# Optimization experiments

Measured on AMD Instinct MI355X. Metric: run time of the kernel, lower is better.

## Reference

```python
import jax, jax.numpy as jnp
import numpy as np

EPS_COS = 1e-8  # torch cosine_similarity eps
EPS_LN = 1e-5   # torch LayerNorm eps


def setup_inputs() -> dict:
    key = jax.random.key(0)
    ks = jax.random.split(key, 8)
    B, N, D, C = 256, 65536, 1024, 103
    s = 1.0 / np.sqrt(D)
    return {
        "visual_input": jnp.zeros((1,), jnp.float32),
        "query_input": jax.random.normal(ks[0], (B, D), jnp.float32),
        "memory_keys": jax.random.normal(ks[1], (N, D), jnp.float32),
        "W_enc": jax.random.normal(ks[2], (D, D), jnp.float32) * s,
        "b_enc": jnp.zeros((D,), jnp.float32),
        "W_d": jax.random.normal(ks[3], (D, D), jnp.float32) * s,
        "b_d": jnp.zeros((D,), jnp.float32),
        "ln_g": jnp.ones((D,), jnp.float32),
        "ln_b": jnp.zeros((D,), jnp.float32),
        "W_cls": jax.random.normal(ks[4], (C, 2 * D), jnp.float32) * (1.0 / np.sqrt(2 * D)),
        "b_cls": jnp.zeros((C,), jnp.float32),
        "k": 32,
    }


def reference(visual_input, query_input, memory_keys, W_enc, b_enc, W_d, b_d,
              ln_g, ln_b, W_cls, b_cls, k):
    # visual encoder + relu -> query embedding [B, D]
    q = jax.nn.relu(query_input @ W_enc.T + b_enc)
    # cosine-similarity kNN over memory bank [N, D]
    qn = q / jnp.maximum(jnp.linalg.norm(q, axis=-1, keepdims=True), EPS_COS)
    mn = memory_keys / jnp.maximum(jnp.linalg.norm(memory_keys, axis=-1, keepdims=True), EPS_COS)
    sim = qn @ mn.T                      # [B, N]
    _, idx = jax.lax.top_k(sim, k)       # [B, k]
    mk = memory_keys[idx]                # [B, k, D] gather
    # memory attention
    qt = jax.nn.relu(q @ W_d.T + b_d)    # [B, D]
    scores = jnp.einsum('bd,bkd->bk', qt, mk)
    w = jax.nn.softmax(scores, axis=-1)
    attended = jnp.einsum('bk,bkd->bd', w, mk)
    x = attended + q
    mu = jnp.mean(x, axis=-1, keepdims=True)
    var = jnp.mean((x - mu) ** 2, axis=-1, keepdims=True)
    ma_out = (x - mu) * jax.lax.rsqrt(var + EPS_LN) * ln_g + ln_b
    # classifier on concatenated features
    merged = jnp.concatenate([q, ma_out], axis=1)  # [B, 2D]
    return merged @ W_cls.T + b_cls
```

## Files before the change

kernel.cpp:

```cpp
#include <hip/hip_runtime.h>
#include <stdint.h>

typedef unsigned short u16;
typedef unsigned int u32;
typedef __attribute__((ext_vector_type(2))) float f32x2;
typedef __attribute__((ext_vector_type(4))) float f32x4;
typedef __attribute__((ext_vector_type(4))) u32 u32x4;
typedef __attribute__((ext_vector_type(2))) u32 u32x2;
typedef __attribute__((ext_vector_type(8))) short bf16x8;

#define NKEYS 65536
#define DIM 1024
#define BQ 256
#define NCLS 103
#define NCAND 64
#define SROW 40

__device__ __forceinline__ u16 f2bf(float x) {
  u32 u = __float_as_uint(x);
  u = u + 0x7FFFu + ((u >> 16) & 1u);
  return (u16)(u >> 16);
}
__device__ __forceinline__ u32 cvtpk(float lo, float hi) {
  u32 d;
  asm("v_cvt_pk_bf16_f32 %0, %1, %2" : "=v"(d) : "v"(lo), "v"(hi));
  return d;
}

__global__ __launch_bounds__(256) void gemm_nt_f32(
    const float* __restrict__ A, const float* __restrict__ B,
    float* __restrict__ partial)
{
  __shared__ float sAT[2][16][68];
  __shared__ float sBT[2][16][68];
  const int tid = threadIdx.x;
  const int n0 = blockIdx.x * 64;
  const int m0 = blockIdx.y * 64;
  const int kz = blockIdx.z;
  const int r = tid & 63, kq = tid >> 6;
  const int tx = tid & 15, ty = tid >> 4;
  float acc[4][4] = {};

  const float* ag = A + (size_t)(m0 + r) * DIM + kz * 256 + kq * 4;
  const float* bg = B + (size_t)(n0 + r) * DIM + kz * 256 + kq * 4;

  f32x4 av = *(const f32x4*)(ag);
  f32x4 bv = *(const f32x4*)(bg);
#pragma unroll
  for (int i = 0; i < 4; ++i) {
    sAT[0][kq * 4 + i][r] = av[i];
    sBT[0][kq * 4 + i][r] = bv[i];
  }
  __syncthreads();

  for (int kb = 0; kb < 16; ++kb) {
    const int cur = kb & 1;
    if (kb + 1 < 16) {
      av = *(const f32x4*)(ag + (kb + 1) * 16);
      bv = *(const f32x4*)(bg + (kb + 1) * 16);
    }
#pragma unroll
    for (int kk = 0; kk < 16; ++kk) {
      const f32x4 a4 = *(const f32x4*)&sAT[cur][kk][ty * 4];
      const f32x4 b4 = *(const f32x4*)&sBT[cur][kk][tx * 4];
#pragma unroll
      for (int i = 0; i < 4; ++i)
#pragma unroll
        for (int j = 0; j < 4; ++j) acc[i][j] += a4[i] * b4[j];
    }
    if (kb + 1 < 16) {
#pragma unroll
      for (int i = 0; i < 4; ++i) {
        sAT[cur ^ 1][kq * 4 + i][r] = av[i];
        sBT[cur ^ 1][kq * 4 + i][r] = bv[i];
      }
    }
    __syncthreads();
  }
#pragma unroll
  for (int i = 0; i < 4; ++i) {
    f32x4 ov = {acc[i][0], acc[i][1], acc[i][2], acc[i][3]};
    *(f32x4*)(partial + (size_t)kz * 262144u + (size_t)(m0 + ty * 4 + i) * DIM + n0 + tx * 4) = ov;
  }
}

__global__ __launch_bounds__(256) void reduce_bias_relu(
    const float* __restrict__ partial, const float* __restrict__ bias,
    float* __restrict__ outf, u16* __restrict__ outb, const int wbf)
{
  const int i4 = blockIdx.x * 256 + threadIdx.x;
  const int e = i4 * 4;
  const int n = e & (DIM - 1);
  f32x4 s = *(const f32x4*)(partial + e);
  s += *(const f32x4*)(partial + 262144u + e);
  s += *(const f32x4*)(partial + 2u * 262144u + e);
  s += *(const f32x4*)(partial + 3u * 262144u + e);
  s += *(const f32x4*)(bias + n);
#pragma unroll
  for (int i = 0; i < 4; ++i) s[i] = fmaxf(s[i], 0.f);
  *(f32x4*)(outf + e) = s;
  if (wbf) {
    u32x2 h = {cvtpk(s[0], s[1]), cvtpk(s[2], s[3])};
    *(u32x2*)(outb + e) = h;
  }
}

__global__ __launch_bounds__(512) void simgemm(
    const float* __restrict__ keys, const u16* __restrict__ qb,
    u16* __restrict__ sim)
{
  __shared__ u16 sA[2][256 * SROW];
  __shared__ u16 sB[2][128 * SROW];
  __shared__ float snorm[128];
  const int tid = threadIdx.x;
  const int n0 = blockIdx.x * 128;

  const int a_r = tid >> 1;
  const int a_h = (tid & 1) * 16;
  const u16* agp = qb + (size_t)a_r * DIM + a_h;
  const int a_ws = a_r * SROW + a_h;

  const int b_r = tid >> 2;
  const int b_q = (tid & 3) * 8;
  const float* bgp = keys + (size_t)(n0 + b_r) * DIM + b_q;
  const int b_ws = b_r * SROW + b_q;

  const int lane = tid & 63, wave = tid >> 6;
  const int wm = (wave >> 1) * 64;
  const int wn = (wave & 1) * 64;
  const int lr = lane & 15;
  const int lk = (lane >> 4) * 8;
  const int l4 = (lane >> 4) * 4;

  float nrm = 0.f;
  f32x4 acc[4][4];
#pragma unroll
  for (int i = 0; i < 4; ++i)
#pragma unroll
    for (int j = 0; j < 4; ++j) acc[i][j] = (f32x4){0.f, 0.f, 0.f, 0.f};

  f32x4 b00, b01, b10, b11, b20, b21, b30, b31;
  u32x4 a00, a01, a10, a11;

#define LOADB(B0, B1, T) do { \
    B0 = *(const f32x4*)(bgp + (size_t)(T) * 32); \
    B1 = *(const f32x4*)(bgp + (size_t)(T) * 32 + 4); \
  } while (0)
#define LOADA(A0, A1, T) do { \
    A0 = *(const u32x4*)(agp + (size_t)(T) * 32); \
    A1 = *(const u32x4*)(agp + (size_t)(T) * 32 + 8); \
  } while (0)
#define WRITE(B0, B1, A0, A1, BUF) do { \
    nrm += B0[0]*B0[0] + B0[1]*B0[1] + B0[2]*B0[2] + B0[3]*B0[3]; \
    nrm += B1[0]*B1[0] + B1[1]*B1[1] + B1[2]*B1[2] + B1[3]*B1[3]; \
    u32x4 bp; \
    bp.x = cvtpk(B0[0], B0[1]); bp.y = cvtpk(B0[2], B0[3]); \
    bp.z = cvtpk(B1[0], B1[1]); bp.w = cvtpk(B1[2], B1[3]); \
    *(u32x4*)&sB[BUF][b_ws] = bp; \
    *(u32x4*)&sA[BUF][a_ws] = A0; \
    *(u32x4*)&sA[BUF][a_ws + 8] = A1; \
  } while (0)
#define COMPUTE(BUF) do { \
    bf16x8 af[4], bfr[4]; \
    _Pragma("unroll") \
    for (int f = 0; f < 4; ++f) { \
      af[f]  = *(const bf16x8*)&sA[BUF][(wm + f * 16 + lr) * SROW + lk]; \
      bfr[f] = *(const bf16x8*)&sB[BUF][(wn + f * 16 + lr) * SROW + lk]; \
    } \
    _Pragma("unroll") \
    for (int i = 0; i < 4; ++i) \
      _Pragma("unroll") \
      for (int j = 0; j < 4; ++j) \
        acc[i][j] = __builtin_amdgcn_mfma_f32_16x16x32_bf16(af[i], bfr[j], acc[i][j], 0, 0, 0); \
  } while (0)

  LOADB(b00, b01, 0); LOADB(b10, b11, 1); LOADB(b20, b21, 2); LOADB(b30, b31, 3);
  LOADA(a00, a01, 0); LOADA(a10, a11, 1);
  WRITE(b00, b01, a00, a01, 0);
  __syncthreads();

  for (int tt = 0; tt < 32; tt += 4) {
    if (tt + 4 < 32) LOADB(b00, b01, tt + 4);
    LOADA(a00, a01, tt + 2);
    COMPUTE(0);
    WRITE(b10, b11, a10, a11, 1);
    __syncthreads();
    if (tt + 5 < 32) LOADB(b10, b11, tt + 5);
    LOADA(a10, a11, tt + 3);
    COMPUTE(1);
    WRITE(b20, b21, a00, a01, 0);
    __syncthreads();
    if (tt + 6 < 32) LOADB(b20, b21, tt + 6);
    if (tt + 4 < 32) LOADA(a00, a01, tt + 4);
    COMPUTE(0);
    WRITE(b30, b31, a10, a11, 1);
    __syncthreads();
    if (tt + 7 < 32) LOADB(b30, b31, tt + 7);
    if (tt + 5 < 32) LOADA(a10, a11, tt + 5);
    COMPUTE(1);
    if (tt + 4 < 32) WRITE(b00, b01, a00, a01, 0);
    __syncthreads();
  }
#undef LOADB
#undef LOADA
#undef WRITE
#undef COMPUTE

  nrm += __shfl_xor(nrm, 1);
  nrm += __shfl_xor(nrm, 2);
  if ((tid & 3) == 0) snorm[b_r] = nrm;
  __syncthreads();

#pragma unroll
  for (int j = 0; j < 4; ++j) {
    const int nl = wn + j * 16 + lr;
    const float scl = 1.f / fmaxf(sqrtf(snorm[nl]), 1e-8f);
    const size_t ng = (size_t)(n0 + nl);
#pragma unroll
    for (int i = 0; i < 4; ++i) {
      const int mb = wm + i * 16 + l4;
#pragma unroll
      for (int r = 0; r < 4; ++r) {
        sim[(size_t)(mb + r) * NKEYS + ng] = f2bf(acc[i][j][r] * scl);
      }
    }
  }
}

__global__ __launch_bounds__(512) void select_attn_cls(
    const u16* __restrict__ sim, const float* __restrict__ keys,
    const float* __restrict__ q, const float* __restrict__ qt,
    const float* __restrict__ ln_g, const float* __restrict__ ln_b,
    const float* __restrict__ Wc, const float* __restrict__ bc,
    float* __restrict__ out)
{
  __shared__ int redc[8];
  __shared__ int sc1, sc2;
  __shared__ int clist[NCAND];
  __shared__ float sdq[NCAND], sdqt[NCAND], snr[NCAND];
  __shared__ int srowi[32];
  __shared__ float sw[32];
  __shared__ float red1[8], red2[8];
  __shared__ float smg[2048];
  const int tid = threadIdx.x, lane = tid & 63, wave = tid >> 6;
  const int m = blockIdx.x;

  const u32x4* row = (const u32x4*)(sim + (size_t)m * NKEYS);
  u32 ku[16][4];
#pragma unroll
  for (int i = 0; i < 16; ++i) {
    const u32x4 v = row[i * 512 + tid];
#pragma unroll
    for (int c = 0; c < 4; ++c) {
      u32 lo = v[c] & 0xFFFFu, hi = v[c] >> 16;
      lo ^= (lo & 0x8000u) ? 0xFFFFu : 0x8000u;
      hi ^= (hi & 0x8000u) ? 0xFFFFu : 0x8000u;
      ku[i][c] = lo | (hi << 16);
    }
  }
  int lo_b = 0, hi_b = 65536;
  while (hi_b - lo_b > 1) {
    const u32 mid = (u32)((lo_b + hi_b) >> 1);
    int c = 0;
#pragma unroll
    for (int i = 0; i < 16; ++i)
#pragma unroll
      for (int k = 0; k < 4; ++k) {
        const u32 x = ku[i][k];
        c += ((x & 0xFFFFu) >= mid) ? 1 : 0;
        c += ((x >> 16) >= mid) ? 1 : 0;
      }
#pragma unroll
    for (int j = 32; j; j >>= 1) c += __shfl_xor(c, j);
    if ((tid & 63) == 0) redc[tid >> 6] = c;
    __syncthreads();
    int tot = 0;
#pragma unroll
    for (int w = 0; w < 8; ++w) tot += redc[w];
    if (tot >= NCAND) lo_b = (int)mid; else hi_b = (int)mid;
    __syncthreads();
  }
  const u32 tau = (u32)lo_b;

  int ch = 0;
#pragma unroll
  for (int i = 0; i < 16; ++i)
#pragma unroll
    for (int k = 0; k < 4; ++k) {
      const u32 x = ku[i][k];
      ch += ((x & 0xFFFFu) > tau) ? 1 : 0;
      ch += ((x >> 16) > tau) ? 1 : 0;
    }
#pragma unroll
  for (int j = 32; j; j >>= 1) ch += __shfl_xor(ch, j);
  if ((tid & 63) == 0) redc[tid >> 6] = ch;
  if (tid == 0) { sc1 = 0; sc2 = 0; }
  __syncthreads();
  int nhi = 0;
#pragma unroll
  for (int w = 0; w < 8; ++w) nhi += redc[w];

#pragma unroll
  for (int i = 0; i < 16; ++i)
#pragma unroll
    for (int k = 0; k < 4; ++k) {
      const int nb = (i * 512 + tid) * 8 + k * 2;
      const u32 x = ku[i][k];
      const u32 l = x & 0xFFFFu, h = x >> 16;
      if (l > tau) { int p = atomicAdd(&sc1, 1); clist[p] = nb; }
      else if (l == tau) { int p = atomicAdd(&sc2, 1); if (nhi + p < NCAND) clist[nhi + p] = nb; }
      if (h > tau) { int p = atomicAdd(&sc1, 1); clist[p] = nb + 1; }
      else if (h == tau) { int p = atomicAdd(&sc2, 1); if (nhi + p < NCAND) clist[nhi + p] = nb + 1; }
    }
  __syncthreads();

  f32x4 q4[4], qt4[4];
#pragma unroll
  for (int i = 0; i < 4; ++i) {
    q4[i]  = *(const f32x4*)(q  + (size_t)m * DIM + i * 256 + lane * 4);
    qt4[i] = *(const f32x4*)(qt + (size_t)m * DIM + i * 256 + lane * 4);
  }
  for (int ci = 0; ci < 8; ++ci) {
    const int c = wave * 8 + ci;
    const float* kr = keys + (size_t)clist[c] * DIM;
    float dq = 0.f, dt = 0.f, ss = 0.f;
#pragma unroll
    for (int i = 0; i < 4; ++i) {
      const f32x4 kv = *(const f32x4*)(kr + i * 256 + lane * 4);
#pragma unroll
      for (int e = 0; e < 4; ++e) {
        dq += kv[e] * q4[i][e];
        dt += kv[e] * qt4[i][e];
        ss += kv[e] * kv[e];
      }
    }
#pragma unroll
    for (int j = 32; j; j >>= 1) {
      dq += __shfl_xor(dq, j);
      dt += __shfl_xor(dt, j);
      ss += __shfl_xor(ss, j);
    }
    if (lane == 0) { sdq[c] = dq; sdqt[c] = dt; snr[c] = ss; }
  }
  __syncthreads();

  if (wave == 0) {
    float v = sdq[lane] / fmaxf(sqrtf(snr[lane]), 1e-8f);
    int p = lane;
#pragma unroll
    for (int k = 2; k <= 64; k <<= 1)
#pragma unroll
      for (int j = k >> 1; j > 0; j >>= 1) {
        const float ov = __shfl_xor(v, j);
        const int op = __shfl_xor(p, j);
        const bool tl = ((lane & j) == 0) == ((lane & k) == 0);
        const bool take = tl ? (ov > v) : (ov < v);
        if (take) { v = ov; p = op; }
      }
    float sc = (lane < 32) ? sdqt[p] : -3.4e38f;
    float mx = sc;
#pragma unroll
    for (int j = 16; j; j >>= 1) mx = fmaxf(mx, __shfl_xor(mx, j));
    const float e = (lane < 32) ? expf(sc - mx) : 0.f;
    float s = e;
#pragma unroll
    for (int j = 16; j; j >>= 1) s += __shfl_xor(s, j);
    if (lane < 32) { sw[lane] = e / s; srowi[lane] = clist[p]; }
  }
  __syncthreads();

  const int d0 = tid * 2;
  f32x2 at = {0.f, 0.f};
  for (int j = 0; j < 32; ++j) {
    const float wj = sw[j];
    const f32x2 kv = *(const f32x2*)(keys + (size_t)srowi[j] * DIM + d0);
    at += wj * kv;
  }
  const f32x2 qv = *(const f32x2*)(q + (size_t)m * DIM + d0);
  const f32x2 x = at + qv;
  float s1 = x[0] + x[1];
#pragma unroll
  for (int j = 32; j; j >>= 1) s1 += __shfl_xor(s1, j);
  if (lane == 0) red1[wave] = s1;
  __syncthreads();
  float mu = 0.f;
#pragma unroll
  for (int w = 0; w < 8; ++w) mu += red1[w];
  mu *= (1.f / 1024.f);
  const f32x2 xc = x - mu;
  float s2 = xc[0] * xc[0] + xc[1] * xc[1];
#pragma unroll
  for (int j = 32; j; j >>= 1) s2 += __shfl_xor(s2, j);
  if (lane == 0) red2[wave] = s2;
  __syncthreads();
  float var = 0.f;
#pragma unroll
  for (int w = 0; w < 8; ++w) var += red2[w];
  var *= (1.f / 1024.f);
  const float rstd = rsqrtf(var + 1e-5f);
  const f32x2 g = *(const f32x2*)(ln_g + d0);
  const f32x2 b = *(const f32x2*)(ln_b + d0);
  const f32x2 ma = xc * rstd * g + b;
  *(f32x2*)&smg[d0] = qv;
  *(f32x2*)&smg[1024 + d0] = ma;
  __syncthreads();

  for (int c = wave; c < NCLS; c += 8) {
    const float* w = Wc + (size_t)c * 2048;
    float a = 0.f;
#pragma unroll
    for (int i = 0; i < 8; ++i) {
      const f32x4 wv = *(const f32x4*)(w + i * 256 + lane * 4);
      const f32x4 mv = *(const f32x4*)&smg[i * 256 + lane * 4];
#pragma unroll
      for (int e = 0; e < 4; ++e) a += wv[e] * mv[e];
    }
#pragma unroll
    for (int j = 32; j; j >>= 1) a += __shfl_xor(a, j);
    if (lane == 0) out[(size_t)m * NCLS + c] = a + bc[c];
  }
}

extern "C" void kernel_launch(void* const* d_in, const int* in_sizes, int n_in,
                              void* d_out, int out_size, void* d_ws, size_t ws_size,
                              hipStream_t stream)
{
  const float* query = (const float*)d_in[1];
  const float* keys  = (const float*)d_in[2];
  const float* Wenc  = (const float*)d_in[3];
  const float* benc  = (const float*)d_in[4];
  const float* Wd    = (const float*)d_in[5];
  const float* bd    = (const float*)d_in[6];
  const float* lng   = (const float*)d_in[7];
  const float* lnb   = (const float*)d_in[8];
  const float* Wcls  = (const float*)d_in[9];
  const float* bcls  = (const float*)d_in[10];
  float* out = (float*)d_out;
  char* ws = (char*)d_ws;

  float* q   = (float*)(ws + 0);
  float* qt  = (float*)(ws + 1048576u);
  u16*   qb  = (u16*)(ws + 2097152u);
  char*  big = ws + 2621440u;
  float* par = (float*)big;
  u16*   sim = (u16*)big;

  gemm_nt_f32<<<dim3(16, 4, 4), 256, 0, stream>>>(query, Wenc, par);
  reduce_bias_relu<<<256, 256, 0, stream>>>(par, benc, q, qb, 1);
  gemm_nt_f32<<<dim3(16, 4, 4), 256, 0, stream>>>(q, Wd, par);
  reduce_bias_relu<<<256, 256, 0, stream>>>(par, bd, qt, qb, 0);
  simgemm<<<dim3(512), 512, 0, stream>>>(keys, qb, sim);
  select_attn_cls<<<256, 512, 0, stream>>>(sim, keys, q, qt, lng, lnb, Wcls, bcls, out);
}
```

Measured before the change: 183.5 us.

## Fuse qt split-K reduction into select kernel and halve simgemm key tile

The second split-K partial reduction (bias + relu for qt) moves into the selection/attention kernel, which reads the four partial slices per row into shared memory. The separate reduce launch and the qt round trip through global memory go away. The similarity GEMM now uses 64-key tiles across 1024 blocks instead of 128-key tiles across 512, which gives more parallelism. The cost is that the bf16 query tile is reloaded twice as often and each wave has fewer MFMAs to amortise its loads.

```diff
diff --git a/kernel.cpp b/kernel.cpp
--- a/kernel.cpp
+++ b/kernel.cpp
@@ -11,7 +11,6 @@
 
 #define NKEYS 65536
 #define DIM 1024
-#define BQ 256
 #define NCLS 103
 #define NCAND 64
 #define SROW 40
@@ -86,7 +85,7 @@
 
 __global__ __launch_bounds__(256) void reduce_bias_relu(
     const float* __restrict__ partial, const float* __restrict__ bias,
-    float* __restrict__ outf, u16* __restrict__ outb, const int wbf)
+    float* __restrict__ outf, u16* __restrict__ outb)
 {
   const int i4 = blockIdx.x * 256 + threadIdx.x;
   const int e = i4 * 4;
@@ -99,10 +98,8 @@
 #pragma unroll
   for (int i = 0; i < 4; ++i) s[i] = fmaxf(s[i], 0.f);
   *(f32x4*)(outf + e) = s;
-  if (wbf) {
-    u32x2 h = {cvtpk(s[0], s[1]), cvtpk(s[2], s[3])};
-    *(u32x2*)(outb + e) = h;
-  }
+  u32x2 h = {cvtpk(s[0], s[1]), cvtpk(s[2], s[3])};
+  *(u32x2*)(outb + e) = h;
 }
 
 __global__ __launch_bounds__(512) void simgemm(
@@ -110,95 +107,91 @@
     u16* __restrict__ sim)
 {
   __shared__ u16 sA[2][256 * SROW];
-  __shared__ u16 sB[2][128 * SROW];
-  __shared__ float snorm[128];
+  __shared__ u16 sB[2][80 * SROW];
+  __shared__ float snorm[64];
   const int tid = threadIdx.x;
-  const int n0 = blockIdx.x * 128;
+  const int n0 = blockIdx.x * 64;
 
   const int a_r = tid >> 1;
   const int a_h = (tid & 1) * 16;
   const u16* agp = qb + (size_t)a_r * DIM + a_h;
   const int a_ws = a_r * SROW + a_h;
 
-  const int b_r = tid >> 2;
-  const int b_q = (tid & 3) * 8;
+  const int b_r = tid >> 3;
+  const int b_q = (tid & 7) * 4;
   const float* bgp = keys + (size_t)(n0 + b_r) * DIM + b_q;
   const int b_ws = b_r * SROW + b_q;
 
   const int lane = tid & 63, wave = tid >> 6;
   const int wm = (wave >> 1) * 64;
-  const int wn = (wave & 1) * 64;
+  const int wn = (wave & 1) * 32;
   const int lr = lane & 15;
   const int lk = (lane >> 4) * 8;
   const int l4 = (lane >> 4) * 4;
 
   float nrm = 0.f;
-  f32x4 acc[4][4];
+  f32x4 acc[4][2];
 #pragma unroll
   for (int i = 0; i < 4; ++i)
 #pragma unroll
-    for (int j = 0; j < 4; ++j) acc[i][j] = (f32x4){0.f, 0.f, 0.f, 0.f};
-
-  f32x4 b00, b01, b10, b11, b20, b21, b30, b31;
+    for (int j = 0; j < 2; ++j) acc[i][j] = (f32x4){0.f, 0.f, 0.f, 0.f};
+
+  f32x4 bs0, bs1, bs2, bs3;
   u32x4 a00, a01, a10, a11;
 
-#define LOADB(B0, B1, T) do { \
-    B0 = *(const f32x4*)(bgp + (size_t)(T) * 32); \
-    B1 = *(const f32x4*)(bgp + (size_t)(T) * 32 + 4); \
-  } while (0)
+#define LOADB(B0, T) do { B0 = *(const f32x4*)(bgp + (size_t)(T) * 32); } while (0)
 #define LOADA(A0, A1, T) do { \
     A0 = *(const u32x4*)(agp + (size_t)(T) * 32); \
     A1 = *(const u32x4*)(agp + (size_t)(T) * 32 + 8); \
   } while (0)
-#define WRITE(B0, B1, A0, A1, BUF) do { \
+#define WRITE(B0, A0, A1, BUF) do { \
     nrm += B0[0]*B0[0] + B0[1]*B0[1] + B0[2]*B0[2] + B0[3]*B0[3]; \
-    nrm += B1[0]*B1[0] + B1[1]*B1[1] + B1[2]*B1[2] + B1[3]*B1[3]; \
-    u32x4 bp; \
+    u32x2 bp; \
     bp.x = cvtpk(B0[0], B0[1]); bp.y = cvtpk(B0[2], B0[3]); \
-    bp.z = cvtpk(B1[0], B1[1]); bp.w = cvtpk(B1[2], B1[3]); \
-    *(u32x4*)&sB[BUF][b_ws] = bp; \
+    *(u32x2*)&sB[BUF][b_ws] = bp; \
     *(u32x4*)&sA[BUF][a_ws] = A0; \
     *(u32x4*)&sA[BUF][a_ws + 8] = A1; \
   } while (0)
 #define COMPUTE(BUF) do { \
-    bf16x8 af[4], bfr[4]; \
+    bf16x8 af[4], bfr[2]; \
     _Pragma("unroll") \
-    for (int f = 0; f < 4; ++f) { \
+    for (int f = 0; f < 4; ++f) \
       af[f]  = *(const bf16x8*)&sA[BUF][(wm + f * 16 + lr) * SROW + lk]; \
+    _Pragma("unroll") \
+    for (int f = 0; f < 2; ++f) \
       bfr[f] = *(const bf16x8*)&sB[BUF][(wn + f * 16 + lr) * SROW + lk]; \
-    } \
     _Pragma("unroll") \
     for (int i = 0; i < 4; ++i) \
       _Pragma("unroll") \
-      for (int j = 0; j < 4; ++j) \
+      for (int j = 0; j < 2; ++j) \
         acc[i][j] = __builtin_amdgcn_mfma_f32_16x16x32_bf16(af[i], bfr[j], acc[i][j], 0, 0, 0); \
   } while (0)
 
-  LOADB(b00, b01, 0); LOADB(b10, b11, 1); LOADB(b20, b21, 2); LOADB(b30, b31, 3);
+  LOADB(bs0, 0); LOADB(bs1, 1); LOADB(bs2, 2); LOADB(bs3, 3);
   LOADA(a00, a01, 0); LOADA(a10, a11, 1);
-  WRITE(b00, b01, a00, a01, 0);
+  WRITE(bs0, a00, a01, 0);
   __syncthreads();
 
   for (int tt = 0; tt < 32; tt += 4) {
-    if (tt + 4 < 32) LOADB(b00, b01, tt + 4);
+    if (tt + 4 < 32) LOADB(bs0, tt + 4);
     LOADA(a00, a01, tt + 2);
     COMPUTE(0);
-    WRITE(b10, b11, a10, a11, 1);
-    __syncthreads();
-    if (tt + 5 < 32) LOADB(b10, b11, tt + 5);
+    WRITE(bs1, a10, a11, 1);
+    __syncthreads();
+    if (tt + 5 < 32) LOADB(bs1, tt + 5);
     LOADA(a10, a11, tt + 3);
     COMPUTE(1);
-    WRITE(b20, b21, a00, a01, 0);
-    __syncthreads();
-    if (tt + 6 < 32) LOADB(b20, b21, tt + 6);
+    WRITE(bs2, a00, a01, 0);
+    __syncthreads();
+    if (tt + 6 < 32) LOADB(bs2, tt + 6);
     if (tt + 4 < 32) LOADA(a00, a01, tt + 4);
     COMPUTE(0);
-    WRITE(b30, b31, a10, a11, 1);
-    __syncthreads();
-    if (tt + 7 < 32) LOADB(b30, b31, tt + 7);
+    WRITE(bs3, a10, a11, 1);
+    __syncthreads();
+    if (tt + 7 < 32) LOADB(bs3, tt + 7);
     if (tt + 5 < 32) LOADA(a10, a11, tt + 5);
     COMPUTE(1);
-    if (tt + 4 < 32) WRITE(b00, b01, a00, a01, 0);
+    if (tt + 4 < 32) WRITE(bs0, a00, a01, 0);
     __syncthreads();
   }
 #undef LOADB
@@ -208,11 +201,12 @@
 
   nrm += __shfl_xor(nrm, 1);
   nrm += __shfl_xor(nrm, 2);
-  if ((tid & 3) == 0) snorm[b_r] = nrm;
-  __syncthreads();
-
-#pragma unroll
-  for (int j = 0; j < 4; ++j) {
+  nrm += __shfl_xor(nrm, 4);
+  if ((tid & 7) == 0) snorm[b_r] = nrm;
+  __syncthreads();
+
+#pragma unroll
+  for (int j = 0; j < 2; ++j) {
     const int nl = wn + j * 16 + lr;
     const float scl = 1.f / fmaxf(sqrtf(snorm[nl]), 1e-8f);
     const size_t ng = (size_t)(n0 + nl);
@@ -227,13 +221,16 @@
   }
 }
 
-__global__ __launch_bounds__(512) void select_attn_cls(
+__global__ __launch_bounds__(512) void selqt(
     const u16* __restrict__ sim, const float* __restrict__ keys,
-    const float* __restrict__ q, const float* __restrict__ qt,
+    const float* __restrict__ q, const float* __restrict__ par2,
+    const float* __restrict__ bd,
     const float* __restrict__ ln_g, const float* __restrict__ ln_b,
     const float* __restrict__ Wc, const float* __restrict__ bc,
     float* __restrict__ out)
 {
+  __shared__ float sqt[DIM];
+  __shared__ float smg[2048];
   __shared__ int redc[8];
   __shared__ int sc1, sc2;
   __shared__ int clist[NCAND];
@@ -241,9 +238,20 @@
   __shared__ int srowi[32];
   __shared__ float sw[32];
   __shared__ float red1[8], red2[8];
-  __shared__ float smg[2048];
   const int tid = threadIdx.x, lane = tid & 63, wave = tid >> 6;
   const int m = blockIdx.x;
+
+  {
+    const int e = tid * 2;
+    f32x2 s = *(const f32x2*)(par2 + (size_t)m * DIM + e);
+    s += *(const f32x2*)(par2 + 262144u + (size_t)m * DIM + e);
+    s += *(const f32x2*)(par2 + 2u * 262144u + (size_t)m * DIM + e);
+    s += *(const f32x2*)(par2 + 3u * 262144u + (size_t)m * DIM + e);
+    s += *(const f32x2*)(bd + e);
+    sqt[e]     = fmaxf(s[0], 0.f);
+    sqt[e + 1] = fmaxf(s[1], 0.f);
+  }
+  __syncthreads();
 
   const u32x4* row = (const u32x4*)(sim + (size_t)m * NKEYS);
   u32 ku[16][4];
@@ -317,8 +325,8 @@
   f32x4 q4[4], qt4[4];
 #pragma unroll
   for (int i = 0; i < 4; ++i) {
-    q4[i]  = *(const f32x4*)(q  + (size_t)m * DIM + i * 256 + lane * 4);
-    qt4[i] = *(const f32x4*)(qt + (size_t)m * DIM + i * 256 + lane * 4);
+    q4[i]  = *(const f32x4*)(q + (size_t)m * DIM + i * 256 + lane * 4);
+    qt4[i] = *(const f32x4*)&sqt[i * 256 + lane * 4];
   }
   for (int ci = 0; ci < 8; ++ci) {
     const int c = wave * 8 + ci;
@@ -399,8 +407,8 @@
   var *= (1.f / 1024.f);
   const float rstd = rsqrtf(var + 1e-5f);
   const f32x2 g = *(const f32x2*)(ln_g + d0);
-  const f32x2 b = *(const f32x2*)(ln_b + d0);
-  const f32x2 ma = xc * rstd * g + b;
+  const f32x2 bb = *(const f32x2*)(ln_b + d0);
+  const f32x2 ma = xc * rstd * g + bb;
   *(f32x2*)&smg[d0] = qv;
   *(f32x2*)&smg[1024 + d0] = ma;
   __syncthreads();
@@ -438,17 +446,16 @@
   float* out = (float*)d_out;
   char* ws = (char*)d_ws;
 
-  float* q   = (float*)(ws + 0);
-  float* qt  = (float*)(ws + 1048576u);
-  u16*   qb  = (u16*)(ws + 2097152u);
-  char*  big = ws + 2621440u;
-  float* par = (float*)big;
-  u16*   sim = (u16*)big;
-
-  gemm_nt_f32<<<dim3(16, 4, 4), 256, 0, stream>>>(query, Wenc, par);
-  reduce_bias_relu<<<256, 256, 0, stream>>>(par, benc, q, qb, 1);
-  gemm_nt_f32<<<dim3(16, 4, 4), 256, 0, stream>>>(q, Wd, par);
-  reduce_bias_relu<<<256, 256, 0, stream>>>(par, bd, qt, qb, 0);
-  simgemm<<<dim3(512), 512, 0, stream>>>(keys, qb, sim);
-  select_attn_cls<<<256, 512, 0, stream>>>(sim, keys, q, qt, lng, lnb, Wcls, bcls, out);
-}
+  float* q    = (float*)(ws + 0);
+  u16*   qb   = (u16*)(ws + 1048576u);
+  char*  big  = ws + 1572864u;
+  u16*   sim  = (u16*)big;
+  float* par1 = (float*)big;
+  float* par2 = (float*)(ws + 35127296u);
+
+  gemm_nt_f32<<<dim3(16, 4, 4), 256, 0, stream>>>(query, Wenc, par1);
+  reduce_bias_relu<<<256, 256, 0, stream>>>(par1, benc, q, qb);
+  gemm_nt_f32<<<dim3(16, 4, 4), 256, 0, stream>>>(q, Wd, par2);
+  simgemm<<<1024, 512, 0, stream>>>(keys, qb, sim);
+  selqt<<<256, 512, 0, stream>>>(sim, keys, q, par2, bd, lng, lnb, Wcls, bcls, out);
+}
```

After: 195.8 us. 6.7% more time.

## Fuse encoder bias/ReLU into GEMM and fold W_d GEMM into similarity kernel tail

Applied to the files above, without the earlier changes.

Replaces the split-K encoder GEMM plus separate reduce kernel with a single full-K GEMM that applies bias, ReLU and the bf16 conversion in its epilogue. The second GEMM (q @ W_d) is removed as its own launch and computed as a tail stage of each similarity-GEMM block, reusing the shared memory through a union. This cuts the launch count from six to three and drops the partial-sum buffer round trips. The cost is a serial tail on every similarity block and a smaller encoder grid (128 blocks) with a longer K loop.

```diff
diff --git a/kernel.cpp b/kernel.cpp
--- a/kernel.cpp
+++ b/kernel.cpp
@@ -11,7 +11,6 @@
 
 #define NKEYS 65536
 #define DIM 1024
-#define BQ 256
 #define NCLS 103
 #define NCAND 64
 #define SROW 40
@@ -27,91 +26,89 @@
   return d;
 }
 
-__global__ __launch_bounds__(256) void gemm_nt_f32(
+__global__ __launch_bounds__(256) void gemm1f(
     const float* __restrict__ A, const float* __restrict__ B,
-    float* __restrict__ partial)
+    const float* __restrict__ bias, float* __restrict__ outf,
+    u16* __restrict__ outb)
 {
-  __shared__ float sAT[2][16][68];
-  __shared__ float sBT[2][16][68];
+  __shared__ float sAT[2][32][34];
+  __shared__ float sBT[2][32][66];
   const int tid = threadIdx.x;
   const int n0 = blockIdx.x * 64;
-  const int m0 = blockIdx.y * 64;
-  const int kz = blockIdx.z;
-  const int r = tid & 63, kq = tid >> 6;
+  const int m0 = blockIdx.y * 32;
   const int tx = tid & 15, ty = tid >> 4;
-  float acc[4][4] = {};
-
-  const float* ag = A + (size_t)(m0 + r) * DIM + kz * 256 + kq * 4;
-  const float* bg = B + (size_t)(n0 + r) * DIM + kz * 256 + kq * 4;
-
-  f32x4 av = *(const f32x4*)(ag);
-  f32x4 bv = *(const f32x4*)(bg);
+  const int am = tid & 31, ak = (tid >> 5) * 4;
+  const int bn = tid & 63, bk = (tid >> 6) * 8;
+  const float* ag = A + (size_t)(m0 + am) * DIM + ak;
+  const float* bg = B + (size_t)(n0 + bn) * DIM + bk;
+  float acc[2][4] = {};
+
+  f32x4 av = *(const f32x4*)ag;
+  f32x4 bv0 = *(const f32x4*)bg;
+  f32x4 bv1 = *(const f32x4*)(bg + 4);
 #pragma unroll
   for (int i = 0; i < 4; ++i) {
-    sAT[0][kq * 4 + i][r] = av[i];
-    sBT[0][kq * 4 + i][r] = bv[i];
-  }
-  __syncthreads();
-
-  for (int kb = 0; kb < 16; ++kb) {
+    sAT[0][ak + i][am] = av[i];
+    sBT[0][bk + i][bn] = bv0[i];
+    sBT[0][bk + 4 + i][bn] = bv1[i];
+  }
+  __syncthreads();
+
+  for (int kb = 0; kb < 32; ++kb) {
     const int cur = kb & 1;
-    if (kb + 1 < 16) {
-      av = *(const f32x4*)(ag + (kb + 1) * 16);
-      bv = *(const f32x4*)(bg + (kb + 1) * 16);
-    }
-#pragma unroll
-    for (int kk = 0; kk < 16; ++kk) {
-      const f32x4 a4 = *(const f32x4*)&sAT[cur][kk][ty * 4];
+    if (kb + 1 < 32) {
+      av  = *(const f32x4*)(ag + (kb + 1) * 32);
+      bv0 = *(const f32x4*)(bg + (kb + 1) * 32);
+      bv1 = *(const f32x4*)(bg + (kb + 1) * 32 + 4);
+    }
+#pragma unroll
+    for (int kk = 0; kk < 32; ++kk) {
+      const f32x2 a2 = *(const f32x2*)&sAT[cur][kk][ty * 2];
       const f32x4 b4 = *(const f32x4*)&sBT[cur][kk][tx * 4];
 #pragma unroll
-      for (int i = 0; i < 4; ++i)
-#pragma unroll
-        for (int j = 0; j < 4; ++j) acc[i][j] += a4[i] * b4[j];
-    }
-    if (kb + 1 < 16) {
+      for (int i = 0; i < 2; ++i)
+#pragma unroll
+        for (int j = 0; j < 4; ++j) acc[i][j] += a2[i] * b4[j];
+    }
+    if (kb + 1 < 32) {
 #pragma unroll
       for (int i = 0; i < 4; ++i) {
-        sAT[cur ^ 1][kq * 4 + i][r] = av[i];
-        sBT[cur ^ 1][kq * 4 + i][r] = bv[i];
-      }
-    }
-    __syncthreads();
-  }
-#pragma unroll
-  for (int i = 0; i < 4; ++i) {
-    f32x4 ov = {acc[i][0], acc[i][1], acc[i][2], acc[i][3]};
-    *(f32x4*)(partial + (size_t)kz * 262144u + (size_t)(m0 + ty * 4 + i) * DIM + n0 + tx * 4) = ov;
-  }
-}
-
-__global__ __launch_bounds__(256) void reduce_bias_relu(
-    const float* __restrict__ partial, const float* __restrict__ bias,
-    float* __restrict__ outf, u16* __restrict__ outb, const int wbf)
+        sAT[cur ^ 1][ak + i][am] = av[i];
+        sBT[cur ^ 1][bk + i][bn] = bv0[i];
+        sBT[cur ^ 1][bk + 4 + i][bn] = bv1[i];
+      }
+    }
+    __syncthreads();
+  }
+
+#pragma unroll
+  for (int i = 0; i < 2; ++i) {
+    const int m = m0 + ty * 2 + i;
+    const int n = n0 + tx * 4;
+    f32x4 s = {acc[i][0], acc[i][1], acc[i][2], acc[i][3]};
+    s += *(const f32x4*)(bias + n);
+#pragma unroll
+    for (int e = 0; e < 4; ++e) s[e] = fmaxf(s[e], 0.f);
+    *(f32x4*)(outf + (size_t)m * DIM + n) = s;
+    u32x2 h = {cvtpk(s[0], s[1]), cvtpk(s[2], s[3])};
+    *(u32x2*)(outb + (size_t)m * DIM + n) = h;
+  }
+}
+
+union SimSmem {
+  struct { u16 sA[2][256 * SROW]; u16 sB[2][128 * SROW]; float snorm[128]; } s;
+  struct { float sA2[2][32][20]; float sB2[2][32][36]; } g;
+};
+
+__global__ __launch_bounds__(512) void simgemm2(
+    const float* __restrict__ keys, const u16* __restrict__ qb,
+    const float* __restrict__ q, const float* __restrict__ Wd,
+    const float* __restrict__ bd, u16* __restrict__ sim,
+    float* __restrict__ qt)
 {
-  const int i4 = blockIdx.x * 256 + threadIdx.x;
-  const int e = i4 * 4;
-  const int n = e & (DIM - 1);
-  f32x4 s = *(const f32x4*)(partial + e);
-  s += *(const f32x4*)(partial + 262144u + e);
-  s += *(const f32x4*)(partial + 2u * 262144u + e);
-  s += *(const f32x4*)(partial + 3u * 262144u + e);
-  s += *(const f32x4*)(bias + n);
-#pragma unroll
-  for (int i = 0; i < 4; ++i) s[i] = fmaxf(s[i], 0.f);
-  *(f32x4*)(outf + e) = s;
-  if (wbf) {
-    u32x2 h = {cvtpk(s[0], s[1]), cvtpk(s[2], s[3])};
-    *(u32x2*)(outb + e) = h;
-  }
-}
-
-__global__ __launch_bounds__(512) void simgemm(
-    const float* __restrict__ keys, const u16* __restrict__ qb,
-    u16* __restrict__ sim)
-{
-  __shared__ u16 sA[2][256 * SROW];
-  __shared__ u16 sB[2][128 * SROW];
-  __shared__ float snorm[128];
+  __shared__ SimSmem sm;
+  u16 (&lsA)[2][256 * SROW] = sm.s.sA;
+  u16 (&lsB)[2][128 * SROW] = sm.s.sB;
   const int tid = threadIdx.x;
   const int n0 = blockIdx.x * 128;
 
@@ -156,16 +153,16 @@
     u32x4 bp; \
     bp.x = cvtpk(B0[0], B0[1]); bp.y = cvtpk(B0[2], B0[3]); \
     bp.z = cvtpk(B1[0], B1[1]); bp.w = cvtpk(B1[2], B1[3]); \
-    *(u32x4*)&sB[BUF][b_ws] = bp; \
-    *(u32x4*)&sA[BUF][a_ws] = A0; \
-    *(u32x4*)&sA[BUF][a_ws + 8] = A1; \
+    *(u32x4*)&lsB[BUF][b_ws] = bp; \
+    *(u32x4*)&lsA[BUF][a_ws] = A0; \
+    *(u32x4*)&lsA[BUF][a_ws + 8] = A1; \
   } while (0)
 #define COMPUTE(BUF) do { \
     bf16x8 af[4], bfr[4]; \
     _Pragma("unroll") \
     for (int f = 0; f < 4; ++f) { \
-      af[f]  = *(const bf16x8*)&sA[BUF][(wm + f * 16 + lr) * SROW + lk]; \
-      bfr[f] = *(const bf16x8*)&sB[BUF][(wn + f * 16 + lr) * SROW + lk]; \
+      af[f]  = *(const bf16x8*)&lsA[BUF][(wm + f * 16 + lr) * SROW + lk]; \
+      bfr[f] = *(const bf16x8*)&lsB[BUF][(wn + f * 16 + lr) * SROW + lk]; \
     } \
     _Pragma("unroll") \
     for (int i = 0; i < 4; ++i) \
@@ -208,13 +205,13 @@
 
   nrm += __shfl_xor(nrm, 1);
   nrm += __shfl_xor(nrm, 2);
-  if ((tid & 3) == 0) snorm[b_r] = nrm;
+  if ((tid & 3) == 0) sm.s.snorm[b_r] = nrm;
   __syncthreads();
 
 #pragma unroll
   for (int j = 0; j < 4; ++j) {
     const int nl = wn + j * 16 + lr;
-    const float scl = 1.f / fmaxf(sqrtf(snorm[nl]), 1e-8f);
+    const float scl = 1.f / fmaxf(sqrtf(sm.s.snorm[nl]), 1e-8f);
     const size_t ng = (size_t)(n0 + nl);
 #pragma unroll
     for (int i = 0; i < 4; ++i) {
@@ -224,6 +221,49 @@
         sim[(size_t)(mb + r) * NKEYS + ng] = f2bf(acc[i][j][r] * scl);
       }
     }
+  }
+  __syncthreads();
+
+  {
+    float (&sA2)[2][32][20] = sm.g.sA2;
+    float (&sB2)[2][32][36] = sm.g.sB2;
+    const int bm = (int)blockIdx.x >> 5;
+    const int bn2 = (int)blockIdx.x & 31;
+    const int om = tid >> 5;
+    const int on = tid & 31;
+    const int sar = tid >> 5, sak = tid & 31;
+    const int sbr = tid >> 4, sbk = (tid & 15) * 2;
+    const float* ag2 = q  + (size_t)(bm * 16 + sar) * DIM + sak;
+    const float* bg2 = Wd + (size_t)(bn2 * 32 + sbr) * DIM + sbk;
+    float accq = 0.f;
+
+    sA2[0][sak][sar] = *ag2;
+    {
+      f32x2 b2 = *(const f32x2*)bg2;
+      sB2[0][sbk][sbr] = b2[0];
+      sB2[0][sbk + 1][sbr] = b2[1];
+    }
+    __syncthreads();
+    for (int kb = 0; kb < 32; ++kb) {
+      const int cur = kb & 1;
+      float an = 0.f;
+      f32x2 bn_ = {0.f, 0.f};
+      if (kb + 1 < 32) {
+        an = ag2[(kb + 1) * 32];
+        bn_ = *(const f32x2*)(bg2 + (kb + 1) * 32);
+      }
+#pragma unroll
+      for (int kk = 0; kk < 32; ++kk)
+        accq += sA2[cur][kk][om] * sB2[cur][kk][on];
+      if (kb + 1 < 32) {
+        sA2[cur ^ 1][sak][sar] = an;
+        sB2[cur ^ 1][sbk][sbr] = bn_[0];
+        sB2[cur ^ 1][sbk + 1][sbr] = bn_[1];
+      }
+      __syncthreads();
+    }
+    const int gm = bm * 16 + om, gn = bn2 * 32 + on;
+    qt[(size_t)gm * DIM + gn] = fmaxf(accq + bd[gn], 0.f);
   }
 }
 
@@ -439,16 +479,11 @@
   char* ws = (char*)d_ws;
 
   float* q   = (float*)(ws + 0);
-  float* qt  = (float*)(ws + 1048576u);
-  u16*   qb  = (u16*)(ws + 2097152u);
-  char*  big = ws + 2621440u;
-  float* par = (float*)big;
-  u16*   sim = (u16*)big;
-
-  gemm_nt_f32<<<dim3(16, 4, 4), 256, 0, stream>>>(query, Wenc, par);
-  reduce_bias_relu<<<256, 256, 0, stream>>>(par, benc, q, qb, 1);
-  gemm_nt_f32<<<dim3(16, 4, 4), 256, 0, stream>>>(q, Wd, par);
-  reduce_bias_relu<<<256, 256, 0, stream>>>(par, bd, qt, qb, 0);
-  simgemm<<<dim3(512), 512, 0, stream>>>(keys, qb, sim);
+  u16*   qb  = (u16*)(ws + 1048576u);
+  float* qt  = (float*)(ws + 1572864u);
+  u16*   sim = (u16*)(ws + 2621440u);
+
+  gemm1f<<<dim3(16, 8), 256, 0, stream>>>(query, Wenc, benc, q, qb);
+  simgemm2<<<512, 512, 0, stream>>>(keys, qb, q, Wd, bd, sim, qt);
   select_attn_cls<<<256, 512, 0, stream>>>(sim, keys, q, qt, lng, lnb, Wcls, bcls, out);
 }
```

Measured after the change: 245.8 us. 34.0% more time.
